# Kernel tuning notes

Measured on AMD Instinct MI355X. Metric: run time of the kernel, lower is better.

The kernel has to match this reference:

```python
import jax, jax.numpy as jnp
import numpy as np

# Winograd F(4x4, 3x3) transform matrices (wincnn convention, as in jiecaoyu/winograd)
BT = jnp.array([
    [4.,  0., -5.,  0., 1., 0.],
    [0., -4., -4.,  1., 1., 0.],
    [0.,  4., -4., -1., 1., 0.],
    [0., -2., -1.,  2., 1., 0.],
    [0.,  2., -1., -2., 1., 0.],
    [0.,  4.,  0., -5., 0., 1.]], dtype=jnp.float32)  # [6,6]
AT = jnp.array([
    [1., 1.,  1., 1.,  1., 0.],
    [0., 1., -1., 2., -2., 0.],
    [0., 1.,  1., 4.,  4., 0.],
    [0., 1., -1., 8., -8., 1.]], dtype=jnp.float32)  # [4,6]

KERNEL = 3
PAD = 1
GROUPS = 1
TILE_IN = 6   # input_tile_size
TILE_OUT = 4  # output_tile_size


def setup_inputs() -> dict:
    key = jax.random.key(0)
    k1, k2, k3 = jax.random.split(key, 3)
    N, Cin, H, W = 16, 64, 128, 128
    Cout = 64
    x = jax.random.normal(k1, (N, Cin, H, W), dtype=jnp.float32)
    # weight is stored in the Winograd (6x6 spectral) domain, as in the module
    weight = jax.random.normal(k2, (Cout, Cin // GROUPS, TILE_IN, TILE_IN), dtype=jnp.float32) * 0.01
    bias = jax.random.normal(k3, (Cout,), dtype=jnp.float32) * 0.01
    return {"x": x, "weight": weight, "bias": bias}


def reference(x, weight, bias):
    N, Cin, H0, W0 = x.shape
    Cout = weight.shape[0]
    g = GROUPS
    # conv padding
    x = jnp.pad(x, ((0, 0), (0, 0), (PAD, PAD), (PAD, PAD)))
    H = x.shape[2]
    out_w = H - KERNEL + 1
    # pad so output width is a multiple of the output tile size
    extra = (-out_w) % TILE_OUT
    if extra:
        x = jnp.pad(x, ((0, 0), (0, 0), (0, extra), (0, extra)))
    nt = (x.shape[2] - TILE_IN) // TILE_OUT + 1  # tiles per spatial dim
    # extract overlapping 6x6 tiles with stride 4 (the torch unfold)
    idx = jnp.arange(nt)[:, None] * TILE_OUT + jnp.arange(TILE_IN)[None, :]  # [nt,6]
    tiles = x[:, :, idx]                 # [N,C,nt,6,Wp]
    tiles = tiles[:, :, :, :, idx]       # [N,C,nt,6,nt,6]
    # input transform: V = BT @ d @ BT^T per tile -> [N,C,nt,nt,6,6]
    V = jnp.einsum('ai,ncpiqj,bj->ncpqab', BT, tiles, BT)
    # grouped spectral GEMM over input channels
    Vg = V.reshape(N, g, Cin // g, nt, nt, TILE_IN, TILE_IN)
    Wg = weight.reshape(g, Cout // g, Cin // g, TILE_IN, TILE_IN)
    M = jnp.einsum('goiab,ngipqab->ngopqab', Wg, Vg)
    M = M.reshape(N, Cout, nt, nt, TILE_IN, TILE_IN)
    # output transform: Y = AT @ M @ AT^T per tile -> [N,O,nt,nt,4,4]
    Y = jnp.einsum('xa,nopqab,yb->nopqxy', AT, M, AT)
    # stitch tiles back: [N,O,nt,4,nt,4] -> [N,O,nt*4,nt*4]
    y = Y.transpose(0, 1, 2, 4, 3, 5).reshape(N, Cout, nt * TILE_OUT, nt * TILE_OUT)
    y = y + bias[None, :, None, None]
    # crop the extra padding
    y = y[:, :, :out_w, :out_w]
    return y
```

## Files before the change

### kernel.cpp

```cpp
#include <hip/hip_runtime.h>
#include <stdint.h>

typedef __attribute__((ext_vector_type(4))) float f32x4;
typedef __attribute__((ext_vector_type(2))) float f32x2;
typedef __attribute__((ext_vector_type(8))) short s16x8;

#define WB_BYTES 294912

__device__ __forceinline__ short f2bf(float f) {
    uint32_t u = __builtin_bit_cast(uint32_t, f);
    u = u + 0x7FFFu + ((u >> 16) & 1u);
    return (short)(u >> 16);
}

__device__ __forceinline__ f32x4 load4u(const float* p) {
    f32x4 v;
    __builtin_memcpy(&v, p, 16);
    return v;
}

__global__ __launch_bounds__(256) void wtrans(const float* __restrict__ wf, short* __restrict__ wb) {
    int tid = blockIdx.x * 256 + threadIdx.x;
    const float* src = wf + tid * 36;
    float w[36];
#pragma unroll
    for (int i = 0; i < 9; i++) {
        f32x4 v = *(const f32x4*)(src + 4 * i);
        w[4*i+0] = v[0]; w[4*i+1] = v[1]; w[4*i+2] = v[2]; w[4*i+3] = v[3];
    }
#pragma unroll
    for (int ab = 0; ab < 36; ab++) wb[ab * 4096 + tid] = f2bf(w[ab]);
}

#define XCI 436
__global__ __launch_bounds__(1024) void wino_fused(const float* __restrict__ x,
                                                   const short* __restrict__ wb,
                                                   const float* __restrict__ bias,
                                                   float* __restrict__ out) {
    __shared__ __align__(16) float SM[32768];
    float* X = SM;
    short* Vs = (short*)(SM + 13952);
    float* P0 = SM;
    float* P1 = SM + 16384;

    int t = threadIdx.x;
    int lane = t & 63;
    int w = t >> 6;
    int cog = w >> 2;
    int grp = w & 3;
    int sh = grp >> 1;
    int bh = grp & 1;
    int lo = lane & 15;
    int kq = lane >> 4;

    int ci_t = t & 31;
    int tl_t = (t >> 5) & 15;
    int s2_t = t >> 9;
    int tp = tl_t >> 2, tq = tl_t & 3;

    int b = blockIdx.x;
    int n = b >> 6, sb = b & 63;
    int p0_ = (sb >> 3) * 4;
    int q0_ = (sb & 7) * 4;
    const float* xb = x + (size_t)n * 64 * 16384;
    int row0 = 4 * p0_ - 1;
    int gc0 = 4 * q0_ - 1;
    int sr = sb >> 3, sc = sb & 7;
    bool interior = (sr >= 1) & (sr <= 6) & (sc >= 1) & (sc <= 6);

    float bv = bias[cog * 16 + kq * 4 + grp];

    f32x4 acc[9];
#pragma unroll
    for (int i = 0; i < 9; i++) acc[i] = (f32x4){0.f, 0.f, 0.f, 0.f};

#pragma unroll
    for (int r = 0; r < 2; r++) {
        const float* xrb = xb + (size_t)r * 32 * 16384;
        if (interior) {
#pragma unroll
            for (int i = 0; i < 4; i++) {
                if (i < 3 || t < 384) {
                    int s = i * 1024 + t;
                    int ci = s / 108;
                    int rem = s - ci * 108;
                    int row = rem / 6;
                    int c4 = rem - row * 6;
                    f32x4 v = load4u(xrb + (size_t)(ci * 128 + row0 + row) * 128 + (gc0 + 4 * c4));
                    *(f32x4*)&X[ci * XCI + row * 24 + c4 * 4] = v;
                }
            }
        } else {
#pragma unroll
            for (int i = 0; i < 4; i++) {
                if (i < 3 || t < 384) {
                    int s = i * 1024 + t;
                    int ci = s / 108;
                    int rem = s - ci * 108;
                    int row = rem / 6;
                    int c4 = rem - row * 6;
                    int gr = row0 + row;
                    int gc = gc0 + 4 * c4;
                    f32x4 v = (f32x4){0.f, 0.f, 0.f, 0.f};
                    if ((unsigned)gr < 128u) {
                        const float* rowp = xrb + (size_t)(ci * 128 + gr) * 128;
                        if (gc >= 0 && gc <= 124) {
                            v = load4u(rowp + gc);
                        } else {
                            if ((unsigned)(gc + 0) < 128u) v[0] = rowp[gc + 0];
                            if ((unsigned)(gc + 1) < 128u) v[1] = rowp[gc + 1];
                            if ((unsigned)(gc + 2) < 128u) v[2] = rowp[gc + 2];
                            if ((unsigned)(gc + 3) < 128u) v[3] = rowp[gc + 3];
                        }
                    }
                    *(f32x4*)&X[ci * XCI + row * 24 + c4 * 4] = v;
                }
            }
        }
        __syncthreads();

        {
            const float* Xb = X + ci_t * XCI + tp * 96 + tq * 4;
            f32x4 ra[5]; f32x2 rb[5];
#pragma unroll
            for (int k = 0; k < 5; k++) {
                int off = (s2_t + k) * 24;
                ra[k] = *(const f32x4*)(Xb + off);
                rb[k] = *(const f32x2*)(Xb + off + 4);
            }
            float Ua[3][6];
#pragma unroll
            for (int c = 0; c < 6; c++) {
                float e0 = (c < 4) ? ra[0][c] : rb[0][c - 4];
                float e1 = (c < 4) ? ra[1][c] : rb[1][c - 4];
                float e2 = (c < 4) ? ra[2][c] : rb[2][c - 4];
                float e3 = (c < 4) ? ra[3][c] : rb[3][c - 4];
                float e4 = (c < 4) ? ra[4][c] : rb[4][c - 4];
                if (s2_t == 0) {
                    float e = fmaf(-4.f, e2, e4);
                    float f = fmaf(-4.f, e1, e3);
                    Ua[0][c] = fmaf(4.f, e0 - e2, e4 - e2);
                    Ua[1][c] = e + f;
                    Ua[2][c] = e - f;
                } else {
                    float g = e3 - e1;
                    float h = e2 - e0;
                    Ua[0][c] = fmaf(2.f, h, g);
                    Ua[1][c] = fmaf(-2.f, h, g);
                    Ua[2][c] = fmaf(4.f, e0 - e2, e4 - e2);
                }
            }
            short* vb = Vs + tl_t * 40 + ci_t;
#pragma unroll
            for (int ar = 0; ar < 3; ar++) {
                float m0 = Ua[ar][0], m1 = Ua[ar][1], m2 = Ua[ar][2];
                float m3 = Ua[ar][3], m4 = Ua[ar][4], m5 = Ua[ar][5];
                float e = fmaf(-4.f, m2, m4);
                float f = fmaf(-4.f, m1, m3);
                float g = m4 - m2;
                float h = m3 - m1;
                int base = (s2_t * 3 + ar) * 6;
                vb[(base + 0) * 640] = f2bf(fmaf(4.f, m0 - m2, g));
                vb[(base + 1) * 640] = f2bf(e + f);
                vb[(base + 2) * 640] = f2bf(e - f);
                vb[(base + 3) * 640] = f2bf(fmaf(2.f, h, g));
                vb[(base + 4) * 640] = f2bf(fmaf(-2.f, h, g));
                vb[(base + 5) * 640] = f2bf(fmaf(4.f, m1 - m3, m5 - m3));
            }
        }
        __syncthreads();

        {
            const short* wb_base = wb + (cog * 16 + lo) * 64 + r * 32 + kq * 8;
            const short* v_base = Vs + lo * 40 + kq * 8;
#pragma unroll
            for (int ar = 0; ar < 3; ar++) {
#pragma unroll
                for (int br = 0; br < 3; br++) {
                    int ab = (3 * sh + ar) * 6 + 3 * bh + br;
                    s16x8 a0 = *(const s16x8*)(wb_base + ab * 4096);
                    s16x8 b0 = *(const s16x8*)(v_base + ab * 640);
                    acc[ar * 3 + br] = __builtin_amdgcn_mfma_f32_16x16x32_bf16(a0, b0, acc[ar * 3 + br], 0, 0, 0);
                }
            }
        }
    }

    __syncthreads();
    int p = p0_ + (lo >> 2);
    int q = q0_ + (lo & 3);
    float* Pown = (sh == 0) ? P0 : P1;

    if (bh == 0) {
#pragma unroll
        for (int rr = 0; rr < 4; rr++) {
            float z[4][3];
#pragma unroll
            for (int br = 0; br < 3; br++) {
                float ma = acc[br][rr], mb = acc[3 + br][rr], mc = acc[6 + br][rr];
                if (sh == 0) {
                    float s1 = mb + mc, d1 = mb - mc;
                    z[0][br] = ma + s1; z[1][br] = d1; z[2][br] = s1; z[3][br] = d1;
                } else {
                    float sv = ma + mb, dv = ma - mb;
                    z[0][br] = sv; z[1][br] = 2.f * dv; z[2][br] = 4.f * sv;
                    z[3][br] = fmaf(8.f, dv, mc);
                }
            }
#pragma unroll
            for (int xr = 0; xr < 4; xr++) {
                float s1 = z[xr][1] + z[xr][2], d1 = z[xr][1] - z[xr][2];
                f32x4 y;
                y[0] = z[xr][0] + s1; y[1] = d1; y[2] = s1; y[3] = d1;
                *(f32x4*)&Pown[cog * 4096 + (rr * 4 + xr) * 256 + lane * 4] = y;
            }
        }
    }
    __syncthreads();
    if (bh == 1) {
#pragma unroll
        for (int rr = 0; rr < 4; rr++) {
            float z[4][3];
#pragma unroll
            for (int br = 0; br < 3; br++) {
                float ma = acc[br][rr], mb = acc[3 + br][rr], mc = acc[6 + br][rr];
                if (sh == 0) {
                    float s1 = mb + mc, d1 = mb - mc;
                    z[0][br] = ma + s1; z[1][br] = d1; z[2][br] = s1; z[3][br] = d1;
                } else {
                    float sv = ma + mb, dv = ma - mb;
                    z[0][br] = sv; z[1][br] = 2.f * dv; z[2][br] = 4.f * sv;
                    z[3][br] = fmaf(8.f, dv, mc);
                }
            }
#pragma unroll
            for (int xr = 0; xr < 4; xr++) {
                float s2 = z[xr][0] + z[xr][1], d2 = z[xr][0] - z[xr][1];
                f32x4 y;
                y[0] = s2; y[1] = 2.f * d2; y[2] = 4.f * s2;
                y[3] = fmaf(8.f, d2, z[xr][2]);
                float* pp = &Pown[cog * 4096 + (rr * 4 + xr) * 256 + lane * 4];
                f32x4 old = *(const f32x4*)pp;
                *(f32x4*)pp = old + y;
            }
        }
    }
    __syncthreads();
    {
        int rr = grp;
        int co = cog * 16 + kq * 4 + rr;
        float* ob = out + ((size_t)(n * 64 + co) * 128 + 4 * p) * 128 + 4 * q;
#pragma unroll
        for (int xr = 0; xr < 4; xr++) {
            int idx = cog * 4096 + (rr * 4 + xr) * 256 + lane * 4;
            f32x4 a0 = *(const f32x4*)&P0[idx];
            f32x4 a1 = *(const f32x4*)&P1[idx];
            f32x4 y;
            y[0] = a0[0] + a1[0] + bv;
            y[1] = a0[1] + a1[1] + bv;
            y[2] = a0[2] + a1[2] + bv;
            y[3] = a0[3] + a1[3] + bv;
            *(f32x4*)(ob + xr * 128) = y;
        }
    }
}

extern "C" void kernel_launch(void* const* d_in, const int* in_sizes, int n_in,
                              void* d_out, int out_size, void* d_ws, size_t ws_size,
                              hipStream_t stream) {
    const float* x    = (const float*)d_in[0];
    const float* wf   = (const float*)d_in[1];
    const float* bias = (const float*)d_in[2];
    float* out = (float*)d_out;

    if (ws_size < WB_BYTES) return;
    short* wb = (short*)d_ws;

    wtrans<<<16, 256, 0, stream>>>(wf, wb);
    wino_fused<<<1024, 1024, 0, stream>>>(x, wb, bias, out);
}
```

Baseline: 187.1 us.

## Make wino_fused persistent over four tiles with register-prefetched input loads

The grid shrinks from 1024 to 256 blocks, and each block loops over four virtual tile-blocks. Global input loads for the next half-channel chunk or next tile go into registers before the current GEMM step, so global latency overlaps MFMA work. This also amortises block launch and setup. In exchange it adds register pressure from the prefetch buffer, keeps the many barriers per iteration, and with only 256 blocks of 1024 threads it may not fill all CUs on the device.

```diff
diff --git a/kernel.cpp b/kernel.cpp
--- a/kernel.cpp
+++ b/kernel.cpp
@@ -58,25 +58,21 @@
     int s2_t = t >> 9;
     int tp = tl_t >> 2, tq = tl_t & 3;
 
-    int b = blockIdx.x;
-    int n = b >> 6, sb = b & 63;
-    int p0_ = (sb >> 3) * 4;
-    int q0_ = (sb & 7) * 4;
-    const float* xb = x + (size_t)n * 64 * 16384;
-    int row0 = 4 * p0_ - 1;
-    int gc0 = 4 * q0_ - 1;
-    int sr = sb >> 3, sc = sb & 7;
-    bool interior = (sr >= 1) & (sr <= 6) & (sc >= 1) & (sc <= 6);
-
     float bv = bias[cog * 16 + kq * 4 + grp];
 
     f32x4 acc[9];
 #pragma unroll
     for (int i = 0; i < 9; i++) acc[i] = (f32x4){0.f, 0.f, 0.f, 0.f};
 
-#pragma unroll
-    for (int r = 0; r < 2; r++) {
-        const float* xrb = xb + (size_t)r * 32 * 16384;
+    f32x4 L[4];
+
+    auto issueLoads = [&](int vid, int r) {
+        int n = vid >> 6, sb = vid & 63;
+        int row0 = (sb >> 3) * 16 - 1;
+        int gc0 = (sb & 7) * 16 - 1;
+        int sr = sb >> 3, sc = sb & 7;
+        bool interior = (sr >= 1) & (sr <= 6) & (sc >= 1) & (sc <= 6);
+        const float* xrb = x + ((size_t)n * 64 + r * 32) * 16384;
         if (interior) {
 #pragma unroll
             for (int i = 0; i < 4; i++) {
@@ -86,8 +82,7 @@
                     int rem = s - ci * 108;
                     int row = rem / 6;
                     int c4 = rem - row * 6;
-                    f32x4 v = load4u(xrb + (size_t)(ci * 128 + row0 + row) * 128 + (gc0 + 4 * c4));
-                    *(f32x4*)&X[ci * XCI + row * 24 + c4 * 4] = v;
+                    L[i] = load4u(xrb + (size_t)(ci * 128 + row0 + row) * 128 + (gc0 + 4 * c4));
                 }
             }
         } else {
@@ -113,155 +108,196 @@
                             if ((unsigned)(gc + 3) < 128u) v[3] = rowp[gc + 3];
                         }
                     }
-                    *(f32x4*)&X[ci * XCI + row * 24 + c4 * 4] = v;
-                }
-            }
-        }
-        __syncthreads();
-
+                    L[i] = v;
+                }
+            }
+        }
+    };
+
+    auto writeX = [&]() {
+#pragma unroll
+        for (int i = 0; i < 4; i++) {
+            if (i < 3 || t < 384) {
+                int s = i * 1024 + t;
+                int ci = s / 108;
+                int rem = s - ci * 108;
+                int row = rem / 6;
+                int c4 = rem - row * 6;
+                *(f32x4*)&X[ci * XCI + row * 24 + c4 * 4] = L[i];
+            }
+        }
+    };
+
+    auto transform = [&]() {
+        const float* Xb = X + ci_t * XCI + tp * 96 + tq * 4;
+        f32x4 ra[5]; f32x2 rb[5];
+#pragma unroll
+        for (int k = 0; k < 5; k++) {
+            int off = (s2_t + k) * 24;
+            ra[k] = *(const f32x4*)(Xb + off);
+            rb[k] = *(const f32x2*)(Xb + off + 4);
+        }
+        float Ua[3][6];
+#pragma unroll
+        for (int c = 0; c < 6; c++) {
+            float e0 = (c < 4) ? ra[0][c] : rb[0][c - 4];
+            float e1 = (c < 4) ? ra[1][c] : rb[1][c - 4];
+            float e2 = (c < 4) ? ra[2][c] : rb[2][c - 4];
+            float e3 = (c < 4) ? ra[3][c] : rb[3][c - 4];
+            float e4 = (c < 4) ? ra[4][c] : rb[4][c - 4];
+            if (s2_t == 0) {
+                float e = fmaf(-4.f, e2, e4);
+                float f = fmaf(-4.f, e1, e3);
+                Ua[0][c] = fmaf(4.f, e0 - e2, e4 - e2);
+                Ua[1][c] = e + f;
+                Ua[2][c] = e - f;
+            } else {
+                float g = e3 - e1;
+                float h = e2 - e0;
+                Ua[0][c] = fmaf(2.f, h, g);
+                Ua[1][c] = fmaf(-2.f, h, g);
+                Ua[2][c] = fmaf(4.f, e0 - e2, e4 - e2);
+            }
+        }
+        short* vb = Vs + tl_t * 40 + ci_t;
+#pragma unroll
+        for (int ar = 0; ar < 3; ar++) {
+            float m0 = Ua[ar][0], m1 = Ua[ar][1], m2 = Ua[ar][2];
+            float m3 = Ua[ar][3], m4 = Ua[ar][4], m5 = Ua[ar][5];
+            float e = fmaf(-4.f, m2, m4);
+            float f = fmaf(-4.f, m1, m3);
+            float g = m4 - m2;
+            float h = m3 - m1;
+            int base = (s2_t * 3 + ar) * 6;
+            vb[(base + 0) * 640] = f2bf(fmaf(4.f, m0 - m2, g));
+            vb[(base + 1) * 640] = f2bf(e + f);
+            vb[(base + 2) * 640] = f2bf(e - f);
+            vb[(base + 3) * 640] = f2bf(fmaf(2.f, h, g));
+            vb[(base + 4) * 640] = f2bf(fmaf(-2.f, h, g));
+            vb[(base + 5) * 640] = f2bf(fmaf(4.f, m1 - m3, m5 - m3));
+        }
+    };
+
+    auto gemmStep = [&](int r) {
+        const short* wb_base = wb + (cog * 16 + lo) * 64 + r * 32 + kq * 8;
+        const short* v_base = Vs + lo * 40 + kq * 8;
+#pragma unroll
+        for (int ar = 0; ar < 3; ar++) {
+#pragma unroll
+            for (int br = 0; br < 3; br++) {
+                int ab = (3 * sh + ar) * 6 + 3 * bh + br;
+                s16x8 a0 = *(const s16x8*)(wb_base + ab * 4096);
+                s16x8 b0 = *(const s16x8*)(v_base + ab * 640);
+                acc[ar * 3 + br] = __builtin_amdgcn_mfma_f32_16x16x32_bf16(a0, b0, acc[ar * 3 + br], 0, 0, 0);
+            }
+        }
+    };
+
+    int pb = blockIdx.x;
+    int vidBase = (pb & 7) * 128 + (pb >> 3) * 4;
+
+    issueLoads(vidBase, 0);
+
+#pragma unroll 1
+    for (int it = 0; it < 4; ++it) {
+        int vid = vidBase + it;
+        int n = vid >> 6, sb = vid & 63;
+        int p0_ = (sb >> 3) * 4;
+        int q0_ = (sb & 7) * 4;
+
+        if (it) __syncthreads();
+        writeX();
+        __syncthreads();
+        transform();
+        __syncthreads();
+        issueLoads(vid, 1);
+        gemmStep(0);
+        writeX();
+        __syncthreads();
+        transform();
+        __syncthreads();
+        if (it < 3) issueLoads(vid + 1, 0);
+        gemmStep(1);
+        __syncthreads();
+
+        int p = p0_ + (lo >> 2);
+        int q = q0_ + (lo & 3);
+        float* Pown = (sh == 0) ? P0 : P1;
+
+        if (bh == 0) {
+#pragma unroll
+            for (int rr = 0; rr < 4; rr++) {
+                float z[4][3];
+#pragma unroll
+                for (int br = 0; br < 3; br++) {
+                    float ma = acc[br][rr], mb = acc[3 + br][rr], mc = acc[6 + br][rr];
+                    if (sh == 0) {
+                        float s1 = mb + mc, d1 = mb - mc;
+                        z[0][br] = ma + s1; z[1][br] = d1; z[2][br] = s1; z[3][br] = d1;
+                    } else {
+                        float sv = ma + mb, dv = ma - mb;
+                        z[0][br] = sv; z[1][br] = 2.f * dv; z[2][br] = 4.f * sv;
+                        z[3][br] = fmaf(8.f, dv, mc);
+                    }
+                }
+#pragma unroll
+                for (int xr = 0; xr < 4; xr++) {
+                    float s1 = z[xr][1] + z[xr][2], d1 = z[xr][1] - z[xr][2];
+                    f32x4 y;
+                    y[0] = z[xr][0] + s1; y[1] = d1; y[2] = s1; y[3] = d1;
+                    *(f32x4*)&Pown[cog * 4096 + (rr * 4 + xr) * 256 + lane * 4] = y;
+                }
+            }
+        }
+        __syncthreads();
+        if (bh == 1) {
+#pragma unroll
+            for (int rr = 0; rr < 4; rr++) {
+                float z[4][3];
+#pragma unroll
+                for (int br = 0; br < 3; br++) {
+                    float ma = acc[br][rr], mb = acc[3 + br][rr], mc = acc[6 + br][rr];
+                    if (sh == 0) {
+                        float s1 = mb + mc, d1 = mb - mc;
+                        z[0][br] = ma + s1; z[1][br] = d1; z[2][br] = s1; z[3][br] = d1;
+                    } else {
+                        float sv = ma + mb, dv = ma - mb;
+                        z[0][br] = sv; z[1][br] = 2.f * dv; z[2][br] = 4.f * sv;
+                        z[3][br] = fmaf(8.f, dv, mc);
+                    }
+                }
+#pragma unroll
+                for (int xr = 0; xr < 4; xr++) {
+                    float s2 = z[xr][0] + z[xr][1], d2 = z[xr][0] - z[xr][1];
+                    f32x4 y;
+                    y[0] = s2; y[1] = 2.f * d2; y[2] = 4.f * s2;
+                    y[3] = fmaf(8.f, d2, z[xr][2]);
+                    float* pp = &Pown[cog * 4096 + (rr * 4 + xr) * 256 + lane * 4];
+                    f32x4 old = *(const f32x4*)pp;
+                    *(f32x4*)pp = old + y;
+                }
+            }
+        }
+        __syncthreads();
         {
-            const float* Xb = X + ci_t * XCI + tp * 96 + tq * 4;
-            f32x4 ra[5]; f32x2 rb[5];
-#pragma unroll
-            for (int k = 0; k < 5; k++) {
-                int off = (s2_t + k) * 24;
-                ra[k] = *(const f32x4*)(Xb + off);
-                rb[k] = *(const f32x2*)(Xb + off + 4);
-            }
-            float Ua[3][6];
-#pragma unroll
-            for (int c = 0; c < 6; c++) {
-                float e0 = (c < 4) ? ra[0][c] : rb[0][c - 4];
-                float e1 = (c < 4) ? ra[1][c] : rb[1][c - 4];
-                float e2 = (c < 4) ? ra[2][c] : rb[2][c - 4];
-                float e3 = (c < 4) ? ra[3][c] : rb[3][c - 4];
-                float e4 = (c < 4) ? ra[4][c] : rb[4][c - 4];
-                if (s2_t == 0) {
-                    float e = fmaf(-4.f, e2, e4);
-                    float f = fmaf(-4.f, e1, e3);
-                    Ua[0][c] = fmaf(4.f, e0 - e2, e4 - e2);
-                    Ua[1][c] = e + f;
-                    Ua[2][c] = e - f;
-                } else {
-                    float g = e3 - e1;
-                    float h = e2 - e0;
-                    Ua[0][c] = fmaf(2.f, h, g);
-                    Ua[1][c] = fmaf(-2.f, h, g);
-                    Ua[2][c] = fmaf(4.f, e0 - e2, e4 - e2);
-                }
-            }
-            short* vb = Vs + tl_t * 40 + ci_t;
-#pragma unroll
-            for (int ar = 0; ar < 3; ar++) {
-                float m0 = Ua[ar][0], m1 = Ua[ar][1], m2 = Ua[ar][2];
-                float m3 = Ua[ar][3], m4 = Ua[ar][4], m5 = Ua[ar][5];
-                float e = fmaf(-4.f, m2, m4);
-                float f = fmaf(-4.f, m1, m3);
-                float g = m4 - m2;
-                float h = m3 - m1;
-                int base = (s2_t * 3 + ar) * 6;
-                vb[(base + 0) * 640] = f2bf(fmaf(4.f, m0 - m2, g));
-                vb[(base + 1) * 640] = f2bf(e + f);
-                vb[(base + 2) * 640] = f2bf(e - f);
-                vb[(base + 3) * 640] = f2bf(fmaf(2.f, h, g));
-                vb[(base + 4) * 640] = f2bf(fmaf(-2.f, h, g));
-                vb[(base + 5) * 640] = f2bf(fmaf(4.f, m1 - m3, m5 - m3));
-            }
-        }
-        __syncthreads();
-
-        {
-            const short* wb_base = wb + (cog * 16 + lo) * 64 + r * 32 + kq * 8;
-            const short* v_base = Vs + lo * 40 + kq * 8;
-#pragma unroll
-            for (int ar = 0; ar < 3; ar++) {
-#pragma unroll
-                for (int br = 0; br < 3; br++) {
-                    int ab = (3 * sh + ar) * 6 + 3 * bh + br;
-                    s16x8 a0 = *(const s16x8*)(wb_base + ab * 4096);
-                    s16x8 b0 = *(const s16x8*)(v_base + ab * 640);
-                    acc[ar * 3 + br] = __builtin_amdgcn_mfma_f32_16x16x32_bf16(a0, b0, acc[ar * 3 + br], 0, 0, 0);
-                }
-            }
-        }
-    }
-
-    __syncthreads();
-    int p = p0_ + (lo >> 2);
-    int q = q0_ + (lo & 3);
-    float* Pown = (sh == 0) ? P0 : P1;
-
-    if (bh == 0) {
-#pragma unroll
-        for (int rr = 0; rr < 4; rr++) {
-            float z[4][3];
-#pragma unroll
-            for (int br = 0; br < 3; br++) {
-                float ma = acc[br][rr], mb = acc[3 + br][rr], mc = acc[6 + br][rr];
-                if (sh == 0) {
-                    float s1 = mb + mc, d1 = mb - mc;
-                    z[0][br] = ma + s1; z[1][br] = d1; z[2][br] = s1; z[3][br] = d1;
-                } else {
-                    float sv = ma + mb, dv = ma - mb;
-                    z[0][br] = sv; z[1][br] = 2.f * dv; z[2][br] = 4.f * sv;
-                    z[3][br] = fmaf(8.f, dv, mc);
-                }
-            }
+            int rr = grp;
+            int co = cog * 16 + kq * 4 + rr;
+            float* ob = out + ((size_t)(n * 64 + co) * 128 + 4 * p) * 128 + 4 * q;
 #pragma unroll
             for (int xr = 0; xr < 4; xr++) {
-                float s1 = z[xr][1] + z[xr][2], d1 = z[xr][1] - z[xr][2];
+                int idx = cog * 4096 + (rr * 4 + xr) * 256 + lane * 4;
+                f32x4 a0 = *(const f32x4*)&P0[idx];
+                f32x4 a1 = *(const f32x4*)&P1[idx];
                 f32x4 y;
-                y[0] = z[xr][0] + s1; y[1] = d1; y[2] = s1; y[3] = d1;
-                *(f32x4*)&Pown[cog * 4096 + (rr * 4 + xr) * 256 + lane * 4] = y;
-            }
-        }
-    }
-    __syncthreads();
-    if (bh == 1) {
-#pragma unroll
-        for (int rr = 0; rr < 4; rr++) {
-            float z[4][3];
-#pragma unroll
-            for (int br = 0; br < 3; br++) {
-                float ma = acc[br][rr], mb = acc[3 + br][rr], mc = acc[6 + br][rr];
-                if (sh == 0) {
-                    float s1 = mb + mc, d1 = mb - mc;
-                    z[0][br] = ma + s1; z[1][br] = d1; z[2][br] = s1; z[3][br] = d1;
-                } else {
-                    float sv = ma + mb, dv = ma - mb;
-                    z[0][br] = sv; z[1][br] = 2.f * dv; z[2][br] = 4.f * sv;
-                    z[3][br] = fmaf(8.f, dv, mc);
-                }
-            }
-#pragma unroll
-            for (int xr = 0; xr < 4; xr++) {
-                float s2 = z[xr][0] + z[xr][1], d2 = z[xr][0] - z[xr][1];
-                f32x4 y;
-                y[0] = s2; y[1] = 2.f * d2; y[2] = 4.f * s2;
-                y[3] = fmaf(8.f, d2, z[xr][2]);
-                float* pp = &Pown[cog * 4096 + (rr * 4 + xr) * 256 + lane * 4];
-                f32x4 old = *(const f32x4*)pp;
-                *(f32x4*)pp = old + y;
-            }
-        }
-    }
-    __syncthreads();
-    {
-        int rr = grp;
-        int co = cog * 16 + kq * 4 + rr;
-        float* ob = out + ((size_t)(n * 64 + co) * 128 + 4 * p) * 128 + 4 * q;
-#pragma unroll
-        for (int xr = 0; xr < 4; xr++) {
-            int idx = cog * 4096 + (rr * 4 + xr) * 256 + lane * 4;
-            f32x4 a0 = *(const f32x4*)&P0[idx];
-            f32x4 a1 = *(const f32x4*)&P1[idx];
-            f32x4 y;
-            y[0] = a0[0] + a1[0] + bv;
-            y[1] = a0[1] + a1[1] + bv;
-            y[2] = a0[2] + a1[2] + bv;
-            y[3] = a0[3] + a1[3] + bv;
-            *(f32x4*)(ob + xr * 128) = y;
-        }
+                y[0] = a0[0] + a1[0] + bv;
+                y[1] = a0[1] + a1[1] + bv;
+                y[2] = a0[2] + a1[2] + bv;
+                y[3] = a0[3] + a1[3] + bv;
+                *(f32x4*)(ob + xr * 128) = y;
+            }
+        }
+#pragma unroll
+        for (int i = 0; i < 9; i++) acc[i] = (f32x4){0.f, 0.f, 0.f, 0.f};
     }
 }
 
@@ -277,5 +313,5 @@
     short* wb = (short*)d_ws;
 
     wtrans<<<16, 256, 0, stream>>>(wf, wb);
-    wino_fused<<<1024, 1024, 0, stream>>>(x, wb, bias, out);
-}
+    wino_fused<<<256, 1024, 0, stream>>>(x, wb, bias, out);
+}
```

New measurement: 235.7 us. 26.0% more time.
